# Performance work log

Hardware: AMD Instinct MI355X
Metric: run time of the kernel (lower is better)

The kernel has to match this reference:

```python
import jax, jax.numpy as jnp
import numpy as np
from jax import lax

# dims: batch, seq_len, d_model, heads, d_ff, num_scales, compression_ratio
B, L, D, H, F, S, CR = 4, 1024, 1024, 16, 4096, 4, 2


def setup_inputs() -> dict:
    key = jax.random.key(0)
    ks = jax.random.split(key, 12)
    def rn(k, shape, s=0.02):
        return jax.random.normal(k, shape, dtype=jnp.float32) * s
    return {
        'x': jax.random.normal(ks[0], (B, L, D), dtype=jnp.float32),
        'W_dc': rn(ks[1], (D, D, 3)),            # dilated conv kernel (OIH)
        'b_dc': jnp.zeros((D,), jnp.float32),
        'W_dec': rn(ks[2], (S - 1, D, D, CR)),    # strided decomposition convs
        'Wq': rn(ks[3], (S, D, D)),               # per-scale query proj
        'Wk': rn(ks[4], (S, D, D)),               # per-scale key proj
        'Wv': rn(ks[5], (D, D)),                  # shared value proj
        'Wo': rn(ks[6], (D, D)),                  # shared output proj
        'agg_logits': rn(ks[7], (S,), 1.0),       # convex aggregation logits
        'gamma1': jnp.ones((D,), jnp.float32), 'beta1': jnp.zeros((D,), jnp.float32),
        'gamma2': jnp.ones((D,), jnp.float32), 'beta2': jnp.zeros((D,), jnp.float32),
        'W1': rn(ks[8], (D, F)), 'b1': jnp.zeros((F,), jnp.float32),
        'W2': rn(ks[9], (F, D)), 'b2': jnp.zeros((D,), jnp.float32),
    }


def _conv1d(x_blc, w_oik, stride, pad, rdil):
    # x: [B, L, Cin] -> [B, L', Cout]; w: [Cout, Cin, K]
    y = lax.conv_general_dilated(
        x_blc.transpose(0, 2, 1), w_oik, (stride,), [(pad, pad)],
        rhs_dilation=(rdil,), dimension_numbers=('NCH', 'OIH', 'NCH'))
    return y.transpose(0, 2, 1)


def _ln(x, g, b, eps=1e-5):
    mu = x.mean(-1, keepdims=True)
    v = x.var(-1, keepdims=True)
    return (x - mu) * lax.rsqrt(v + eps) * g + b


def reference(x, W_dc, b_dc, W_dec, Wq, Wk, Wv, Wo, agg_logits,
              gamma1, beta1, gamma2, beta2, W1, b1, W2, b2):
    dh = D // H
    inv_sqrt_dh = 1.0 / jnp.sqrt(jnp.float32(dh))
    residual = x
    # 1. dilated conv (k=3, dil=2, pad=2 -> same length) + ReLU (dropout=eval/identity)
    xc = jax.nn.relu(_conv1d(x, W_dc, 1, 2, 2) + b_dc)
    # 2. hierarchical decomposition: strided convs halving seq length per scale
    scales = [xc]
    for s in range(S - 1):
        scales.append(_conv1d(scales[-1], W_dec[s], CR, 0, 1))
    # 3. multiscale attention: full-res queries attend to each compressed scale;
    #    value projection Wv shared across scales
    outs = []
    for s in range(S):
        Ls = scales[s].shape[1]
        q = (xc @ Wq[s]).reshape(B, L, H, dh)
        k = (scales[s] @ Wk[s]).reshape(B, Ls, H, dh)
        v = (scales[s] @ Wv).reshape(B, Ls, H, dh)
        att = jax.nn.softmax(jnp.einsum('bqhd,bkhd->bhqk', q, k) * inv_sqrt_dh, axis=-1)
        o = jnp.einsum('bhqk,bkhd->bqhd', att, v).reshape(B, L, D) @ Wo
        outs.append(o)
    # 4. convex (optimization-driven) aggregation + entropy sparsity aux loss
    w = jax.nn.softmax(agg_logits)
    maha = jnp.einsum('s,sbld->bld', w, jnp.stack(outs))
    aux_loss = -jnp.sum(w * jnp.log(w + 1e-9))
    # 5. residual + LN + FFN (exact GELU, as torch nn.GELU default)
    x1 = _ln(residual + maha, gamma1, beta1)
    ffn = jax.nn.gelu(x1 @ W1 + b1, approximate=False) @ W2 + b2
    out = _ln(x1 + ffn, gamma2, beta2)
    return out, aux_loss
```

## Files before the change

kernel.cpp:

```cpp
#include <hip/hip_runtime.h>
#include <cstddef>

#define DB 4
#define DL 1024
#define DD 1024
#define DH 16
#define DF 4096

typedef __attribute__((ext_vector_type(8))) short short8;
typedef __attribute__((ext_vector_type(4))) float float4v;

static __device__ __forceinline__ short f2bf(float f) {
    unsigned u = __float_as_uint(f);
    unsigned r = (u + 0x7FFFu + ((u >> 16) & 1u)) >> 16;
    return (short)r;
}

#define GLOAD_LDS16(gp, lp)                                                          \
    __builtin_amdgcn_global_load_lds(                                                \
        (const __attribute__((address_space(1))) void*)(gp),                         \
        (__attribute__((address_space(3))) void*)(lp), 16, 0, 0)

__global__ __launch_bounds__(256) void prep_all_kernel(
    const float* __restrict__ Wdc, const float* __restrict__ Wdec,
    const float* __restrict__ Wq, const float* __restrict__ Wk,
    const float* __restrict__ Wv, const float* __restrict__ Wo,
    const float* __restrict__ W1, const float* __restrict__ W2,
    const float* __restrict__ x, const float* __restrict__ agg,
    short* __restrict__ wdc_bt, short* __restrict__ wdec_bt,
    short* __restrict__ wq4t, short* __restrict__ wkvt, short* __restrict__ wot,
    short* __restrict__ w1t, short* __restrict__ w2t, short* __restrict__ xpad,
    float* __restrict__ wagg, float* __restrict__ aux) {
    __shared__ float tile[32][33];
    const size_t M1 = 1024 * 1024;
    int blk = blockIdx.x, tid = threadIdx.x;
    if (blk < 12288) {
        int idx = blk * 256 + tid;
        int i = idx & 1023, o = (idx >> 10) & 1023, k = idx >> 20;
        wdc_bt[idx] = f2bf(Wdc[((size_t)o * 1024 + i) * 3 + k]);
        return;
    }
    if (blk < 36864) {
        int idx = (blk - 12288) * 256 + tid;
        int i = idx & 1023, k2 = (idx >> 10) & 1, n = (idx >> 11) & 1023, s = idx >> 21;
        wdec_bt[idx] = f2bf(Wdec[(((size_t)(s * 1024 + n)) * 1024 + i) * 2 + k2]);
        return;
    }
    if (blk < 58368) {
        const float* src; short* dst; int K, N, bx, by;
        if (blk < 50176) {
            int r = blk - 36864;
            int z = r >> 10, rem = r & 1023;
            bx = rem & 31; by = rem >> 5; K = 1024; N = 1024;
            if (z < 4)      { src = Wq + (size_t)z * M1;       dst = wq4t + (size_t)z * M1; }
            else if (z < 8) { src = Wk + (size_t)(z - 4) * M1; dst = wkvt + (size_t)(z - 4) * 2 * M1; }
            else if (z < 12){ src = Wv;                        dst = wkvt + (size_t)(z - 8) * 2 * M1 + M1; }
            else            { src = Wo;                        dst = wot; }
        } else if (blk < 54272) {
            int r = blk - 50176;
            bx = r & 127; by = r >> 7; K = 1024; N = 4096; src = W1; dst = w1t;
        } else {
            int r = blk - 54272;
            bx = r & 31; by = r >> 5; K = 4096; N = 1024; src = W2; dst = w2t;
        }
        int n0 = bx << 5, k0 = by << 5;
        int cc = tid & 31, rr = tid >> 5;
#pragma unroll
        for (int p = 0; p < 4; p++) {
            int kk = (p << 3) + rr;
            tile[kk][cc] = src[(size_t)(k0 + kk) * N + n0 + cc];
        }
        __syncthreads();
#pragma unroll
        for (int p = 0; p < 4; p++) {
            int nn = (p << 3) + rr;
            dst[(size_t)(n0 + nn) * K + k0 + cc] = f2bf(tile[cc][nn]);
        }
        return;
    }
    if (blk < 74816) {
        int idx = (blk - 58368) * 256 + tid;
        int d = idx & 1023;
        int row = (idx >> 10) % 1028;
        int b = (idx >> 10) / 1028;
        int l = row - 2;
        float v = (l >= 0 && l < DL) ? x[((size_t)(b * DL + l)) * DD + d] : 0.f;
        xpad[idx] = f2bf(v);
        return;
    }
    if (tid == 0) {
        float l0 = agg[0], l1 = agg[1], l2 = agg[2], l3 = agg[3];
        float m = fmaxf(fmaxf(l0, l1), fmaxf(l2, l3));
        float e0 = __expf(l0 - m), e1 = __expf(l1 - m);
        float e2 = __expf(l2 - m), e3 = __expf(l3 - m);
        float ssum = e0 + e1 + e2 + e3;
        float w0 = e0 / ssum, w1 = e1 / ssum, w2 = e2 / ssum, w3 = e3 / ssum;
        wagg[0] = w0; wagg[1] = w1; wagg[2] = w2; wagg[3] = w3;
        *aux = -(w0 * logf(w0 + 1e-9f) + w1 * logf(w1 + 1e-9f) +
                 w2 * logf(w2 + 1e-9f) + w3 * logf(w3 + 1e-9f));
    }
}

template <int ACT, int OBF>
__global__ __launch_bounds__(256) void mgemm_kernel(
    const short* __restrict__ A, const short* __restrict__ Bt,
    const float* __restrict__ bias, void* __restrict__ Cv,
    int M, int N, int K) {
    __shared__ short As[128 * 32];
    __shared__ short Bs[128 * 32];
    int tid = threadIdx.x;
    int wave = tid >> 6, lane = tid & 63;
    int lq = lane & 15, quad = lane >> 4;
    int m0 = blockIdx.y << 7, n0 = blockIdx.x << 7;
    int wm = (wave & 1) << 6, wn = (wave >> 1) << 6;
    int r0 = tid >> 2, r1 = (256 + tid) >> 2;
    int kc0 = (tid & 3) << 3;
    const short* Ag0 = A + (size_t)(m0 + r0) * K + kc0;
    const short* Ag1 = A + (size_t)(m0 + r1) * K + kc0;
    const short* Bg0 = Bt + (size_t)(n0 + r0) * K + kc0;
    const short* Bg1 = Bt + (size_t)(n0 + r1) * K + kc0;
    float4v acc[4][4];
#pragma unroll
    for (int mi = 0; mi < 4; mi++)
#pragma unroll
        for (int ni = 0; ni < 4; ni++) acc[mi][ni] = (float4v){0.f, 0.f, 0.f, 0.f};

    for (int k0 = 0; k0 < K; k0 += 32) {
        __syncthreads();
        GLOAD_LDS16(Ag0 + k0, As + tid * 8);
        GLOAD_LDS16(Ag1 + k0, As + (256 + tid) * 8);
        GLOAD_LDS16(Bg0 + k0, Bs + tid * 8);
        GLOAD_LDS16(Bg1 + k0, Bs + (256 + tid) * 8);
        __syncthreads();
        short8 af[4], bfr[4];
#pragma unroll
        for (int mi = 0; mi < 4; mi++)
            af[mi] = *(const short8*)(As + ((wm + (mi << 4) + lq) << 5) + (quad << 3));
#pragma unroll
        for (int ni = 0; ni < 4; ni++)
            bfr[ni] = *(const short8*)(Bs + ((wn + (ni << 4) + lq) << 5) + (quad << 3));
#pragma unroll
        for (int mi = 0; mi < 4; mi++)
#pragma unroll
            for (int ni = 0; ni < 4; ni++)
                acc[mi][ni] = __builtin_amdgcn_mfma_f32_16x16x32_bf16(
                    af[mi], bfr[ni], acc[mi][ni], 0, 0, 0);
    }
#pragma unroll
    for (int ni = 0; ni < 4; ni++) {
        int col = n0 + wn + (ni << 4) + lq;
        float bv = bias ? bias[col] : 0.f;
#pragma unroll
        for (int mi = 0; mi < 4; mi++) {
#pragma unroll
            for (int r = 0; r < 4; r++) {
                int row = m0 + wm + (mi << 4) + (quad << 2) + r;
                float v = acc[mi][ni][r] + bv;
                if (ACT == 1) v = 0.5f * v * (1.0f + erff(v * 0.70710678118654752f));
                if (OBF) ((short*)Cv)[(size_t)row * N + col] = f2bf(v);
                else ((float*)Cv)[(size_t)row * N + col] = v;
            }
        }
    }
}

__global__ __launch_bounds__(256) void kvgemm_kernel(
    const short* __restrict__ acts, const short* __restrict__ wkvt,
    short* __restrict__ kvall, short* __restrict__ kfrall) {
    __shared__ short As[128 * 32];
    __shared__ short Bs[128 * 32];
    int my = blockIdx.y;
    int s = my < 32 ? 0 : my < 48 ? 1 : my < 56 ? 2 : 3;
    int m0 = my << 7;
    int rb = s == 0 ? 0 : s == 1 ? 4096 : s == 2 ? 6144 : 7168;
    size_t doff = s == 0 ? 0 : s == 1 ? 4194304 : s == 2 ? 6291456 : 7340032;
    int Ls = DL >> s;
    const short* Bt = wkvt + (size_t)s * 2097152;
    const int K = 1024, N = 2048;
    int tid = threadIdx.x;
    int wave = tid >> 6, lane = tid & 63;
    int lq = lane & 15, quad = lane >> 4;
    int n0 = blockIdx.x << 7;
    int wm = (wave & 1) << 6, wn = (wave >> 1) << 6;
    int r0 = tid >> 2, r1 = (256 + tid) >> 2;
    int kc0 = (tid & 3) << 3;
    const short* Ag0 = acts + (size_t)(m0 + r0) * K + kc0;
    const short* Ag1 = acts + (size_t)(m0 + r1) * K + kc0;
    const short* Bg0 = Bt + (size_t)(n0 + r0) * K + kc0;
    const short* Bg1 = Bt + (size_t)(n0 + r1) * K + kc0;
    float4v acc[4][4];
#pragma unroll
    for (int mi = 0; mi < 4; mi++)
#pragma unroll
        for (int ni = 0; ni < 4; ni++) acc[mi][ni] = (float4v){0.f, 0.f, 0.f, 0.f};
    for (int k0 = 0; k0 < K; k0 += 32) {
        __syncthreads();
        GLOAD_LDS16(Ag0 + k0, As + tid * 8);
        GLOAD_LDS16(Ag1 + k0, As + (256 + tid) * 8);
        GLOAD_LDS16(Bg0 + k0, Bs + tid * 8);
        GLOAD_LDS16(Bg1 + k0, Bs + (256 + tid) * 8);
        __syncthreads();
        short8 af[4], bfr[4];
#pragma unroll
        for (int mi = 0; mi < 4; mi++)
            af[mi] = *(const short8*)(As + ((wm + (mi << 4) + lq) << 5) + (quad << 3));
#pragma unroll
        for (int ni = 0; ni < 4; ni++)
            bfr[ni] = *(const short8*)(Bs + ((wn + (ni << 4) + lq) << 5) + (quad << 3));
#pragma unroll
        for (int mi = 0; mi < 4; mi++)
#pragma unroll
            for (int ni = 0; ni < 4; ni++)
                acc[mi][ni] = __builtin_amdgcn_mfma_f32_16x16x32_bf16(
                    af[mi], bfr[ni], acc[mi][ni], 0, 0, 0);
    }
    bool isK = (n0 < 1024);
#pragma unroll
    for (int ni = 0; ni < 4; ni++) {
        int col = n0 + wn + (ni << 4) + lq;
        if (isK) {
            int h = col >> 6, dc = (col >> 3) & 7, di = col & 7;
#pragma unroll
            for (int mi = 0; mi < 4; mi++)
#pragma unroll
                for (int r = 0; r < 4; r++) {
                    int row = m0 + wm + (mi << 4) + (quad << 2) + r;
                    int jg = row - rb;
                    int b = jg >> (10 - s);
                    int j = jg & (Ls - 1);
                    int bh = (b << 4) | h;
                    size_t addr = doff + (((size_t)bh * (Ls >> 4) + (j >> 4)) << 10) +
                                  (dc << 7) + ((j & 15) << 3) + di;
                    kfrall[addr] = f2bf(acc[mi][ni][r]);
                }
        } else {
#pragma unroll
            for (int mi = 0; mi < 4; mi++)
#pragma unroll
                for (int r = 0; r < 4; r++) {
                    int row = m0 + wm + (mi << 4) + (quad << 2) + r;
                    kvall[(size_t)row * N + col] = f2bf(acc[mi][ni][r]);
                }
        }
    }
}

__global__ __launch_bounds__(256) void mgemm_pk_kernel(
    const short* __restrict__ A, const short* __restrict__ Bt,
    const float* __restrict__ bias, float* __restrict__ Cout,
    int M, int N, int Kfull, int KH) {
    __shared__ short As[128 * 32];
    __shared__ short Bs[128 * 32];
    int kz = blockIdx.z;
    const short* Ab = A + (size_t)kz * KH;
    const short* Btb = Bt + (size_t)kz * KH;
    float* Co = Cout + (size_t)kz * M * N;
    int tid = threadIdx.x;
    int wave = tid >> 6, lane = tid & 63;
    int lq = lane & 15, quad = lane >> 4;
    int m0 = blockIdx.y << 7, n0 = blockIdx.x << 7;
    int wm = (wave & 1) << 6, wn = (wave >> 1) << 6;
    int r0 = tid >> 2, r1 = (256 + tid) >> 2;
    int kc0 = (tid & 3) << 3;
    const short* Ag0 = Ab + (size_t)(m0 + r0) * Kfull + kc0;
    const short* Ag1 = Ab + (size_t)(m0 + r1) * Kfull + kc0;
    const short* Bg0 = Btb + (size_t)(n0 + r0) * Kfull + kc0;
    const short* Bg1 = Btb + (size_t)(n0 + r1) * Kfull + kc0;
    float4v acc[4][4];
#pragma unroll
    for (int mi = 0; mi < 4; mi++)
#pragma unroll
        for (int ni = 0; ni < 4; ni++) acc[mi][ni] = (float4v){0.f, 0.f, 0.f, 0.f};
    for (int k0 = 0; k0 < KH; k0 += 32) {
        __syncthreads();
        GLOAD_LDS16(Ag0 + k0, As + tid * 8);
        GLOAD_LDS16(Ag1 + k0, As + (256 + tid) * 8);
        GLOAD_LDS16(Bg0 + k0, Bs + tid * 8);
        GLOAD_LDS16(Bg1 + k0, Bs + (256 + tid) * 8);
        __syncthreads();
        short8 af[4], bfr[4];
#pragma unroll
        for (int mi = 0; mi < 4; mi++)
            af[mi] = *(const short8*)(As + ((wm + (mi << 4) + lq) << 5) + (quad << 3));
#pragma unroll
        for (int ni = 0; ni < 4; ni++)
            bfr[ni] = *(const short8*)(Bs + ((wn + (ni << 4) + lq) << 5) + (quad << 3));
#pragma unroll
        for (int mi = 0; mi < 4; mi++)
#pragma unroll
            for (int ni = 0; ni < 4; ni++)
                acc[mi][ni] = __builtin_amdgcn_mfma_f32_16x16x32_bf16(
                    af[mi], bfr[ni], acc[mi][ni], 0, 0, 0);
    }
#pragma unroll
    for (int ni = 0; ni < 4; ni++) {
        int col = n0 + wn + (ni << 4) + lq;
        float bv = (bias && kz == 0) ? bias[col] : 0.f;
#pragma unroll
        for (int mi = 0; mi < 4; mi++)
#pragma unroll
            for (int r = 0; r < 4; r++) {
                int row = m0 + wm + (mi << 4) + (quad << 2) + r;
                Co[(size_t)row * N + col] = acc[mi][ni][r] + bv;
            }
    }
}

__global__ __launch_bounds__(256) void sumcast4_kernel(
    const float* __restrict__ p, size_t stride, short* __restrict__ outp) {
    int idx = (blockIdx.x * 256 + threadIdx.x) << 2;
    float4 a0 = *(const float4*)&p[idx];
    float4 a1 = *(const float4*)&p[stride + idx];
    float4 a2 = *(const float4*)&p[2 * stride + idx];
    float4 a3 = *(const float4*)&p[3 * stride + idx];
    ushort4 u;
    u.x = (unsigned short)f2bf(a0.x + a1.x + a2.x + a3.x);
    u.y = (unsigned short)f2bf(a0.y + a1.y + a2.y + a3.y);
    u.z = (unsigned short)f2bf(a0.z + a1.z + a2.z + a3.z);
    u.w = (unsigned short)f2bf(a0.w + a1.w + a2.w + a3.w);
    *(ushort4*)&outp[idx] = u;
}

__global__ __launch_bounds__(256) void convdil_pk_kernel(
    const short* __restrict__ xp, const short* __restrict__ Wt,
    float* __restrict__ pbuf) {
    __shared__ short As[128 * 32];
    __shared__ short Bs[128 * 32];
    int kp = blockIdx.z;
    int tid = threadIdx.x;
    int wave = tid >> 6, lane = tid & 63;
    int lq = lane & 15, quad = lane >> 4;
    int m0 = blockIdx.y << 7, n0 = blockIdx.x << 7;
    int wm = (wave & 1) << 6, wn = (wave >> 1) << 6;
    int b = m0 >> 10, ll0 = m0 & 1023;
    int r0 = tid >> 2, r1 = (256 + tid) >> 2;
    int kc = (tid & 3) << 3;
    float* Co = pbuf + (size_t)kp * DB * DL * DD;
    const short* Abase = xp + ((size_t)(b * 1028 + ll0 + 2 * kp)) * DD + kc;
    const short* Bbase = Wt + (size_t)kp * DD * DD;
    const short* Bg0 = Bbase + (size_t)(n0 + r0) * DD + kc;
    const short* Bg1 = Bbase + (size_t)(n0 + r1) * DD + kc;
    float4v acc[4][4];
#pragma unroll
    for (int mi = 0; mi < 4; mi++)
#pragma unroll
        for (int ni = 0; ni < 4; ni++) acc[mi][ni] = (float4v){0.f, 0.f, 0.f, 0.f};
    for (int k0 = 0; k0 < DD; k0 += 32) {
        __syncthreads();
        GLOAD_LDS16(Abase + (size_t)r0 * DD + k0, As + tid * 8);
        GLOAD_LDS16(Abase + (size_t)r1 * DD + k0, As + (256 + tid) * 8);
        GLOAD_LDS16(Bg0 + k0, Bs + tid * 8);
        GLOAD_LDS16(Bg1 + k0, Bs + (256 + tid) * 8);
        __syncthreads();
        short8 af[4], bfr[4];
#pragma unroll
        for (int mi = 0; mi < 4; mi++)
            af[mi] = *(const short8*)(As + ((wm + (mi << 4) + lq) << 5) + (quad << 3));
#pragma unroll
        for (int ni = 0; ni < 4; ni++)
            bfr[ni] = *(const short8*)(Bs + ((wn + (ni << 4) + lq) << 5) + (quad << 3));
#pragma unroll
        for (int mi = 0; mi < 4; mi++)
#pragma unroll
            for (int ni = 0; ni < 4; ni++)
                acc[mi][ni] = __builtin_amdgcn_mfma_f32_16x16x32_bf16(
                    af[mi], bfr[ni], acc[mi][ni], 0, 0, 0);
    }
#pragma unroll
    for (int ni = 0; ni < 4; ni++) {
        int col = n0 + wn + (ni << 4) + lq;
#pragma unroll
        for (int mi = 0; mi < 4; mi++)
#pragma unroll
            for (int r = 0; r < 4; r++) {
                int row = m0 + wm + (mi << 4) + (quad << 2) + r;
                Co[(size_t)row * DD + col] = acc[mi][ni][r];
            }
    }
}

__global__ __launch_bounds__(256) void convcomb_kernel(
    const float* __restrict__ pbuf, const float* __restrict__ bvec,
    short* __restrict__ xcb) {
    const size_t M4 = (size_t)DB * DL * DD;
    int idx = (blockIdx.x * 256 + threadIdx.x) << 2;
    int col = idx & 1023;
    float4 p0 = *(const float4*)&pbuf[idx];
    float4 p1 = *(const float4*)&pbuf[M4 + idx];
    float4 p2 = *(const float4*)&pbuf[2 * M4 + idx];
    float4 bb = *(const float4*)&bvec[col];
    ushort4 u;
    u.x = (unsigned short)f2bf(fmaxf(p0.x + p1.x + p2.x + bb.x, 0.f));
    u.y = (unsigned short)f2bf(fmaxf(p0.y + p1.y + p2.y + bb.y, 0.f));
    u.z = (unsigned short)f2bf(fmaxf(p0.z + p1.z + p2.z + bb.z, 0.f));
    u.w = (unsigned short)f2bf(fmaxf(p0.w + p1.w + p2.w + bb.w, 0.f));
    *(ushort4*)&xcb[idx] = u;
}

__global__ __launch_bounds__(256) void vfrag_all_kernel(const short* __restrict__ kvall,
                                                        short* __restrict__ vfr0) {
    __shared__ short tile[32][33];
    int flat = blockIdx.x;
    int s, base, rb;
    size_t doff;
    if (flat < 4096)      { s = 0; base = 0;    rb = 0;    doff = 0; }
    else if (flat < 6144) { s = 1; base = 4096; rb = 4096; doff = 4194304; }
    else if (flat < 7168) { s = 2; base = 6144; rb = 6144; doff = 6291456; }
    else                  { s = 3; base = 7168; rb = 7168; doff = 7340032; }
    int rem = flat - base;
    int Ls = DL >> s;
    int nt = Ls >> 5;
    int j0t = rem & (nt - 1);
    int rest = rem >> (5 - s);
    int dt = rest & 1;
    int bh = rest >> 1;
    int j0 = j0t << 5, d0 = dt << 5;
    int b = bh >> 4, h = bh & 15;
    int tid = threadIdx.x;
    int cc = tid & 31, rr = tid >> 5;
#pragma unroll
    for (int p = 0; p < 4; p++) {
        int jj = (p << 3) + rr;
        tile[jj][cc] = kvall[((size_t)(rb + b * Ls + j0 + jj) << 11) + 1024 +
                             (h << 6) + d0 + cc];
    }
    __syncthreads();
    int c = j0 >> 6, ks = (j0 >> 5) & 1;
#pragma unroll
    for (int p = 0; p < 4; p++) {
        int d = d0 + (p << 3) + rr;
        int tt = d >> 4, lqv = d & 15;
        size_t off = doff + (((size_t)bh * (Ls >> 6) + c) << 12) + (ks << 11) +
                     (tt << 9) + (lqv << 5) + cc;
        vfr0[off] = tile[cc][(p << 3) + rr];
    }
}

__global__ __launch_bounds__(256) void attn_fused6_kernel(
    const short* __restrict__ qb4, const short* __restrict__ kfr0,
    const short* __restrict__ vfr0, const float* __restrict__ wagg,
    short* __restrict__ attb) {
    __shared__ __align__(16) short plds[4][16][72];
    int tid = threadIdx.x;
    int w = tid >> 6, lane = tid & 63;
    int lq = lane & 15, quad = lane >> 4;
    int bh = blockIdx.x;
    int b = bh >> 4, h = bh & 15;
    int qrow0 = b * DL + (blockIdx.y << 6) + (w << 4);
    const float c_exp = 0.18033688f;

    float fin[4][4];
#pragma unroll
    for (int t = 0; t < 4; t++)
#pragma unroll
        for (int r = 0; r < 4; r++) fin[t][r] = 0.f;

#pragma unroll 1
    for (int s = 0; s < 4; s++) {
        int Ls = DL >> s;
        size_t doff = s == 0 ? 0 : s == 1 ? 4194304 : s == 2 ? 6291456 : 7340032;

        const short* qbase = qb4 + ((size_t)(qrow0 + lq) << 12) + (s << 10) +
                             (h << 6) + (quad << 3);
        short8 qf0 = *(const short8*)qbase;
        short8 qf1 = *(const short8*)(qbase + 32);

        const short* kfb = kfr0 + doff + (((size_t)bh * (Ls >> 4)) << 10) +
                           (quad << 7) + (lq << 3);
        const short* vfb = vfr0 + doff + (((size_t)bh * (Ls >> 6)) << 12) +
                           (lq << 5) + (quad << 3);

        float4v O[4];
        float lpart[4] = {0.f, 0.f, 0.f, 0.f};
#pragma unroll
        for (int t = 0; t < 4; t++) O[t] = (float4v){0.f, 0.f, 0.f, 0.f};

        for (int c0 = 0; c0 < Ls; c0 += 64) {
            float4v S[4];
            int g0 = c0 >> 4;
#pragma unroll
            for (int t = 0; t < 4; t++) {
                const short* kp = kfb + ((size_t)(g0 + t) << 10);
                short8 kf0 = *(const short8*)kp;
                short8 kf1 = *(const short8*)(kp + 512);
                float4v z = (float4v){0.f, 0.f, 0.f, 0.f};
                z = __builtin_amdgcn_mfma_f32_16x16x32_bf16(qf0, kf0, z, 0, 0, 0);
                S[t] = __builtin_amdgcn_mfma_f32_16x16x32_bf16(qf1, kf1, z, 0, 0, 0);
            }
#pragma unroll
            for (int t = 0; t < 4; t++)
#pragma unroll
                for (int r = 0; r < 4; r++) {
                    float p = exp2f(S[t][r] * c_exp);
                    lpart[r] += p;
                    plds[w][(quad << 2) + r][(t << 4) + lq] =
                        (short)(__float_as_uint(p) >> 16);
                }
            const short* vcb = vfb + ((size_t)(c0 >> 6) << 12);
#pragma unroll
            for (int ks = 0; ks < 2; ks++) {
                short8 af = *(const short8*)&plds[w][lq][(ks << 5) + (quad << 3)];
#pragma unroll
                for (int t = 0; t < 4; t++) {
                    short8 vf = *(const short8*)(vcb + (ks << 11) + (t << 9));
                    O[t] = __builtin_amdgcn_mfma_f32_16x16x32_bf16(af, vf, O[t], 0, 0, 0);
                }
            }
        }
        float wsc = wagg[s];
#pragma unroll
        for (int r = 0; r < 4; r++) {
            float l = lpart[r];
            l += __shfl_xor(l, 1, 64);
            l += __shfl_xor(l, 2, 64);
            l += __shfl_xor(l, 4, 64);
            l += __shfl_xor(l, 8, 64);
            float linv = wsc / l;
#pragma unroll
            for (int t = 0; t < 4; t++) fin[t][r] += O[t][r] * linv;
        }
    }
#pragma unroll
    for (int r = 0; r < 4; r++) {
        size_t rbase = ((size_t)(qrow0 + (quad << 2) + r) << 10) + (h << 6) + lq;
#pragma unroll
        for (int t = 0; t < 4; t++)
            attb[rbase + (t << 4)] = f2bf(fin[t][r]);
    }
}

template <int NP, int OBF>
__global__ __launch_bounds__(256) void addlnN_kernel(
    const float* __restrict__ a, const float* __restrict__ pb, size_t pstride,
    const float* __restrict__ gam, const float* __restrict__ bet,
    float* __restrict__ out, short* __restrict__ outb) {
    __shared__ float redA[4], redB[4];
    int row = blockIdx.x, tid = threadIdx.x;
    size_t base = (size_t)row * DD + (tid << 2);
    float4 av = *(const float4*)&a[base];
    float s0 = av.x, s1 = av.y, s2 = av.z, s3 = av.w;
#pragma unroll
    for (int j = 0; j < NP; j++) {
        float4 pv = *(const float4*)&pb[(size_t)j * pstride + base];
        s0 += pv.x; s1 += pv.y; s2 += pv.z; s3 += pv.w;
    }
    float lsum = s0 + s1 + s2 + s3;
    float lsq = s0 * s0 + s1 * s1 + s2 * s2 + s3 * s3;
#pragma unroll
    for (int o = 32; o > 0; o >>= 1) {
        lsum += __shfl_down(lsum, o, 64);
        lsq += __shfl_down(lsq, o, 64);
    }
    int lane = tid & 63, wid = tid >> 6;
    if (lane == 0) { redA[wid] = lsum; redB[wid] = lsq; }
    __syncthreads();
    float tsum = redA[0] + redA[1] + redA[2] + redA[3];
    float tsq = redB[0] + redB[1] + redB[2] + redB[3];
    float mean = tsum * (1.0f / DD);
    float var = tsq * (1.0f / DD) - mean * mean;
    float rstd = rsqrtf(var + 1e-5f);
    float4 gv = *(const float4*)&gam[tid << 2];
    float4 bev = *(const float4*)&bet[tid << 2];
    float4 o;
    o.x = (s0 - mean) * rstd * gv.x + bev.x;
    o.y = (s1 - mean) * rstd * gv.y + bev.y;
    o.z = (s2 - mean) * rstd * gv.z + bev.z;
    o.w = (s3 - mean) * rstd * gv.w + bev.w;
    *(float4*)&out[base] = o;
    if (OBF) {
        ushort4 u;
        u.x = (unsigned short)f2bf(o.x);
        u.y = (unsigned short)f2bf(o.y);
        u.z = (unsigned short)f2bf(o.z);
        u.w = (unsigned short)f2bf(o.w);
        *(ushort4*)&outb[base] = u;
    }
}

extern "C" void kernel_launch(void* const* d_in, const int* in_sizes, int n_in,
                              void* d_out, int out_size, void* d_ws, size_t ws_size,
                              hipStream_t stream) {
    (void)in_sizes; (void)n_in; (void)out_size; (void)ws_size;
    const float* x   = (const float*)d_in[0];
    const float* Wdc = (const float*)d_in[1];
    const float* bdc = (const float*)d_in[2];
    const float* Wdec= (const float*)d_in[3];
    const float* Wq  = (const float*)d_in[4];
    const float* Wk  = (const float*)d_in[5];
    const float* Wv  = (const float*)d_in[6];
    const float* Wo  = (const float*)d_in[7];
    const float* agg = (const float*)d_in[8];
    const float* g1  = (const float*)d_in[9];
    const float* be1 = (const float*)d_in[10];
    const float* g2  = (const float*)d_in[11];
    const float* be2 = (const float*)d_in[12];
    const float* W1  = (const float*)d_in[13];
    const float* b1  = (const float*)d_in[14];
    const float* W2  = (const float*)d_in[15];
    const float* b2  = (const float*)d_in[16];
    float* out = (float*)d_out;

    float* ws = (float*)d_ws;
    size_t off = 0;
    auto alloc = [&](size_t nfloats) { float* p = ws + off; off += nfloats; return p; };
    const size_t M1 = 1024 * 1024;
    short* wdc_bt  = (short*)alloc(3 * M1 / 2);
    short* wdec_bt = (short*)alloc(3 * M1);
    short* wq4t    = (short*)alloc(2 * M1);
    short* wkvt    = (short*)alloc(4 * M1);
    short* wot     = (short*)alloc(M1 / 2);
    short* w1t     = (short*)alloc(2 * M1);
    short* w2t     = (short*)alloc(2 * M1);
    float* wagg    = alloc(64);
    short* xpad    = (short*)alloc(2105344);
    short* xcb     = (short*)alloc(2 * M1);
    short* s1b     = (short*)alloc(M1);
    short* s2b     = (short*)alloc(M1 / 2);
    short* s3b     = (short*)alloc(M1 / 4);
    short* qb4     = (short*)alloc(8 * M1);
    short* kvall   = (short*)alloc(7 * M1 + M1 / 2);
    short* kfrall  = (short*)alloc(3 * M1 + 3 * M1 / 4);
    short* vfrall  = (short*)alloc(3 * M1 + 3 * M1 / 4);
    short* attb    = (short*)alloc(2 * M1);
    float* x1      = alloc(4 * M1);
    short* x1b     = (short*)alloc(2 * M1);
    float* pkbuf   = alloc(8 * M1);
    short* hb      = qb4;
    float* convp   = (float*)qb4;
    float* pk4     = (float*)kvall;

    dim3 blk(256);
    prep_all_kernel<<<dim3(74817), blk, 0, stream>>>(
        Wdc, Wdec, Wq, Wk, Wv, Wo, W1, W2, x, agg,
        wdc_bt, wdec_bt, wq4t, wkvt, wot, w1t, w2t, xpad, wagg,
        out + (size_t)DB * DL * DD);

    convdil_pk_kernel<<<dim3(DD / 128, DB * DL / 128, 3), blk, 0, stream>>>(
        xpad, wdc_bt, convp);
    convcomb_kernel<<<dim3(4 * M1 / (256 * 4)), blk, 0, stream>>>(convp, bdc, xcb);

    mgemm_pk_kernel<<<dim3(8, 16, 4), blk, 0, stream>>>(
        xcb, wdec_bt, nullptr, pkbuf, 2048, DD, 2 * DD, 512);
    sumcast4_kernel<<<dim3(2 * M1 / 1024), blk, 0, stream>>>(pkbuf, 2 * M1, s1b);
    mgemm_pk_kernel<<<dim3(8, 8, 4), blk, 0, stream>>>(
        s1b, wdec_bt + 2 * M1, nullptr, pkbuf, 1024, DD, 2 * DD, 512);
    sumcast4_kernel<<<dim3(M1 / 1024), blk, 0, stream>>>(pkbuf, M1, s2b);
    mgemm_pk_kernel<<<dim3(8, 4, 4), blk, 0, stream>>>(
        s2b, wdec_bt + 4 * M1, nullptr, pkbuf, 512, DD, 2 * DD, 512);
    sumcast4_kernel<<<dim3(M1 / 2048), blk, 0, stream>>>(pkbuf, M1 / 2, s3b);

    mgemm_kernel<0, 1><<<dim3(32, 32), blk, 0, stream>>>(
        xcb, wq4t, nullptr, qb4, DB * DL, 4 * DD, DD);

    kvgemm_kernel<<<dim3(16, 60), blk, 0, stream>>>(xcb, wkvt, kvall, kfrall);

    vfrag_all_kernel<<<dim3(7680), blk, 0, stream>>>(kvall, vfrall);

    attn_fused6_kernel<<<dim3(DB * DH, DL / 64), blk, 0, stream>>>(
        qb4, kfrall, vfrall, wagg, attb);

    mgemm_pk_kernel<<<dim3(8, 32, 2), blk, 0, stream>>>(
        attb, wot, nullptr, pkbuf, DB * DL, DD, DD, DD / 2);

    addlnN_kernel<2, 1><<<dim3(DB * DL), blk, 0, stream>>>(
        x, pkbuf, 4 * M1, g1, be1, x1, x1b);

    mgemm_kernel<1, 1><<<dim3(DF / 128, (DB * DL) / 128), blk, 0, stream>>>(
        x1b, w1t, b1, hb, DB * DL, DF, DD);
    mgemm_pk_kernel<<<dim3(8, 32, 4), blk, 0, stream>>>(
        hb, w2t, b2, pk4, DB * DL, DD, DF, DF / 4);

    addlnN_kernel<4, 0><<<dim3(DB * DL), blk, 0, stream>>>(
        x1, pk4, 4 * M1, g2, be2, out, nullptr);
}
```

Baseline: 759.7 us.

## Compute transposed attention scores to keep P in registers, skipping LDS round-trip

The QK^T MFMA operands are swapped so each lane holds score rows in an order that packs directly into the A-operand fragment for the PV MFMA. This removes the per-chunk shared-memory write and read of P. The V fragment layout in vfrag_all is permuted to match the new key ordering, and V loads are issued at the start of each chunk so they overlap with the score compute. The row-sum reduction becomes a single per-lane sum followed by cross-quad shuffles.

Result: no change. 760.8 us (+0.1%).

```diff
diff --git a/kernel.cpp b/kernel.cpp
--- a/kernel.cpp
+++ b/kernel.cpp
@@ -426,21 +426,21 @@
     }
     __syncthreads();
     int c = j0 >> 6, ks = (j0 >> 5) & 1;
+    int pc = (((cc >> 2) & 1) << 4) | ((cc >> 3) << 2) | (cc & 3);
 #pragma unroll
     for (int p = 0; p < 4; p++) {
         int d = d0 + (p << 3) + rr;
         int tt = d >> 4, lqv = d & 15;
         size_t off = doff + (((size_t)bh * (Ls >> 6) + c) << 12) + (ks << 11) +
                      (tt << 9) + (lqv << 5) + cc;
-        vfr0[off] = tile[cc][(p << 3) + rr];
-    }
-}
-
-__global__ __launch_bounds__(256) void attn_fused6_kernel(
+        vfr0[off] = tile[pc][(p << 3) + rr];
+    }
+}
+
+__global__ __launch_bounds__(256) void attn_fused7_kernel(
     const short* __restrict__ qb4, const short* __restrict__ kfr0,
     const short* __restrict__ vfr0, const float* __restrict__ wagg,
     short* __restrict__ attb) {
-    __shared__ __align__(16) short plds[4][16][72];
     int tid = threadIdx.x;
     int w = tid >> 6, lane = tid & 63;
     int lq = lane & 15, quad = lane >> 4;
@@ -471,11 +471,19 @@
                            (lq << 5) + (quad << 3);
 
         float4v O[4];
-        float lpart[4] = {0.f, 0.f, 0.f, 0.f};
+        float lsum = 0.f;
 #pragma unroll
         for (int t = 0; t < 4; t++) O[t] = (float4v){0.f, 0.f, 0.f, 0.f};
 
         for (int c0 = 0; c0 < Ls; c0 += 64) {
+            const short* vcb = vfb + ((size_t)(c0 >> 6) << 12);
+            short8 vf[2][4];
+#pragma unroll
+            for (int ks = 0; ks < 2; ks++)
+#pragma unroll
+                for (int t = 0; t < 4; t++)
+                    vf[ks][t] = *(const short8*)(vcb + (ks << 11) + (t << 9));
+
             float4v S[4];
             int g0 = c0 >> 4;
 #pragma unroll
@@ -483,39 +491,47 @@
                 const short* kp = kfb + ((size_t)(g0 + t) << 10);
                 short8 kf0 = *(const short8*)kp;
                 short8 kf1 = *(const short8*)(kp + 512);
-                float4v z = (float4v){0.f, 0.f, 0.f, 0.f};
-                z = __builtin_amdgcn_mfma_f32_16x16x32_bf16(qf0, kf0, z, 0, 0, 0);
-                S[t] = __builtin_amdgcn_mfma_f32_16x16x32_bf16(qf1, kf1, z, 0, 0, 0);
+                float4v zz = (float4v){0.f, 0.f, 0.f, 0.f};
+                zz = __builtin_amdgcn_mfma_f32_16x16x32_bf16(kf0, qf0, zz, 0, 0, 0);
+                S[t] = __builtin_amdgcn_mfma_f32_16x16x32_bf16(kf1, qf1, zz, 0, 0, 0);
             }
+
+            unsigned wpk[8];
+#pragma unroll
+            for (int t = 0; t < 4; t++) {
+                float p0 = exp2f(S[t][0] * c_exp);
+                float p1 = exp2f(S[t][1] * c_exp);
+                float p2 = exp2f(S[t][2] * c_exp);
+                float p3 = exp2f(S[t][3] * c_exp);
+                lsum += p0 + p1 + p2 + p3;
+                wpk[2 * t]     = (__float_as_uint(p1) & 0xFFFF0000u) |
+                                 (__float_as_uint(p0) >> 16);
+                wpk[2 * t + 1] = (__float_as_uint(p3) & 0xFFFF0000u) |
+                                 (__float_as_uint(p2) >> 16);
+            }
+
+            union AFU { unsigned u[4]; short8 s8; };
+            AFU af0, af1;
+            af0.u[0] = wpk[0]; af0.u[1] = wpk[1]; af0.u[2] = wpk[2]; af0.u[3] = wpk[3];
+            af1.u[0] = wpk[4]; af1.u[1] = wpk[5]; af1.u[2] = wpk[6]; af1.u[3] = wpk[7];
 #pragma unroll
             for (int t = 0; t < 4; t++)
-#pragma unroll
-                for (int r = 0; r < 4; r++) {
-                    float p = exp2f(S[t][r] * c_exp);
-                    lpart[r] += p;
-                    plds[w][(quad << 2) + r][(t << 4) + lq] =
-                        (short)(__float_as_uint(p) >> 16);
-                }
-            const short* vcb = vfb + ((size_t)(c0 >> 6) << 12);
-#pragma unroll
-            for (int ks = 0; ks < 2; ks++) {
-                short8 af = *(const short8*)&plds[w][lq][(ks << 5) + (quad << 3)];
-#pragma unroll
-                for (int t = 0; t < 4; t++) {
-                    short8 vf = *(const short8*)(vcb + (ks << 11) + (t << 9));
-                    O[t] = __builtin_amdgcn_mfma_f32_16x16x32_bf16(af, vf, O[t], 0, 0, 0);
-                }
-            }
+                O[t] = __builtin_amdgcn_mfma_f32_16x16x32_bf16(af0.s8, vf[0][t],
+                                                               O[t], 0, 0, 0);
+#pragma unroll
+            for (int t = 0; t < 4; t++)
+                O[t] = __builtin_amdgcn_mfma_f32_16x16x32_bf16(af1.s8, vf[1][t],
+                                                               O[t], 0, 0, 0);
         }
+
+        lsum += __shfl_xor(lsum, 16, 64);
+        lsum += __shfl_xor(lsum, 32, 64);
         float wsc = wagg[s];
 #pragma unroll
         for (int r = 0; r < 4; r++) {
-            float l = lpart[r];
-            l += __shfl_xor(l, 1, 64);
-            l += __shfl_xor(l, 2, 64);
-            l += __shfl_xor(l, 4, 64);
-            l += __shfl_xor(l, 8, 64);
-            float linv = wsc / l;
+            int sl = (lane & 48) | (((lane >> 4) << 2) + r);
+            float lr = __shfl(lsum, sl, 64);
+            float linv = wsc / lr;
 #pragma unroll
             for (int t = 0; t < 4; t++) fin[t][r] += O[t][r] * linv;
         }
@@ -656,7 +672,7 @@
 
     vfrag_all_kernel<<<dim3(7680), blk, 0, stream>>>(kvall, vfrall);
 
-    attn_fused6_kernel<<<dim3(DB * DH, DL / 64), blk, 0, stream>>>(
+    attn_fused7_kernel<<<dim3(DB * DH, DL / 64), blk, 0, stream>>>(
         qb4, kfrall, vfrall, wagg, attb);
 
     mgemm_pk_kernel<<<dim3(8, 32, 2), blk, 0, stream>>>(
```
